# Optimization experiments

Hardware: AMD Instinct MI355X
Metric: run time of the kernel (lower is better)

The kernel has to match this reference:

```python
import jax, jax.numpy as jnp
import numpy as np

B, T, N, IN_DIM = 32, 12, 1024, 1
HID, EMB, K, HOR, OUT = 64, 16, 2, 12, 1


def setup_inputs() -> dict:
    key = jax.random.key(0)
    ks = jax.random.split(key, 12)
    s = 0.1
    return {
        "x": jax.random.normal(ks[0], (B, T, N, IN_DIM), jnp.float32),
        "E": jax.random.normal(ks[1], (N, EMB), jnp.float32),
        # layer 1: gate (z,r) and candidate pools; in = IN_DIM + HID
        "Wg1": jax.random.normal(ks[2], (EMB, K, IN_DIM + HID, 2 * HID), jnp.float32) * s,
        "bg1": jax.random.normal(ks[3], (EMB, 2 * HID), jnp.float32) * s,
        "Wc1": jax.random.normal(ks[4], (EMB, K, IN_DIM + HID, HID), jnp.float32) * s,
        "bc1": jax.random.normal(ks[5], (EMB, HID), jnp.float32) * s,
        # layer 2: in = HID + HID
        "Wg2": jax.random.normal(ks[6], (EMB, K, 2 * HID, 2 * HID), jnp.float32) * s,
        "bg2": jax.random.normal(ks[7], (EMB, 2 * HID), jnp.float32) * s,
        "Wc2": jax.random.normal(ks[8], (EMB, K, 2 * HID, HID), jnp.float32) * s,
        "bc2": jax.random.normal(ks[9], (EMB, HID), jnp.float32) * s,
        # Conv2d(1, HOR*OUT, kernel=(1, HID)) == per-node linear HID -> HOR*OUT
        "Wout": jax.random.normal(ks[10], (HOR * OUT, HID), jnp.float32) * s,
        "bout": jnp.zeros((HOR * OUT,), jnp.float32),
    }


def _supports(E):
    # adaptive adjacency from node embeddings + Chebyshev polynomial set
    A = jax.nn.softmax(jax.nn.relu(E @ E.T), axis=1)  # [N, N]
    sup = [jnp.eye(E.shape[0], dtype=E.dtype), A]
    for _ in range(K - 2):
        sup.append(2.0 * (A @ sup[-1]) - sup[-2])
    return jnp.stack(sup[:K])  # [K, N, N]


def _gconv(x, sup, E, Wp, bp):
    # x: [B, N, Ci]; per-node weights generated from embeddings
    xg = jnp.einsum('knm,bmc->bnkc', sup, x)          # [B, N, K, Ci]
    W = jnp.einsum('nd,dkio->nkio', E, Wp)            # [N, K, Ci, Co]
    b = E @ bp                                        # [N, Co]
    return jnp.einsum('bnki,nkio->bno', xg, W) + b


def _layer(xs, sup, E, Wg, bg, Wc, bc):
    # xs: [T, B, N, Ci]; adaptive graph-conv GRU scanned over time
    hid = Wc.shape[-1]

    def step(h, x_t):
        zr = jax.nn.sigmoid(_gconv(jnp.concatenate([x_t, h], -1), sup, E, Wg, bg))
        z, r = jnp.split(zr, 2, axis=-1)
        hc = jnp.tanh(_gconv(jnp.concatenate([x_t, z * h], -1), sup, E, Wc, bc))
        h_new = r * h + (1.0 - r) * hc
        return h_new, h_new

    h0 = jnp.zeros((xs.shape[1], xs.shape[2], hid), xs.dtype)
    _, hs = jax.lax.scan(step, h0, xs)
    return hs  # [T, B, N, hid]


def reference(x, E, Wg1, bg1, Wc1, bc1, Wg2, bg2, Wc2, bc2, Wout, bout):
    sup = _supports(E)
    xs = jnp.swapaxes(x, 0, 1)                        # [T, B, N, in]
    h1 = _layer(xs, sup, E, Wg1, bg1, Wc1, bc1)       # [T, B, N, HID]
    h2 = _layer(h1, sup, E, Wg2, bg2, Wc2, bc2)       # [T, B, N, HID]
    h_last = h2[-1]                                   # [B, N, HID]
    out = jnp.einsum('bnh,oh->bno', h_last, Wout) + bout  # [B, N, HOR*OUT]
    out = jnp.transpose(out, (0, 2, 1)).reshape(x.shape[0], HOR, OUT, N)
    return jnp.transpose(out, (0, 1, 3, 2))           # [B, HOR, N, OUT]
```

## Files before the change

kernel.cpp:

```cpp
#include <hip/hip_runtime.h>
#include <math.h>

#define NN 1024
#define BB 32
#define TTT 12
#define HH 64
#define DD 16

__device__ __forceinline__ float dot4f(const float4 v, const float* __restrict__ wv) {
    return v.x * wv[0] + v.y * wv[1] + v.z * wv[2] + v.w * wv[3];
}

__device__ __forceinline__ float sigmoidf_(float x) { return 1.0f / (1.0f + expf(-x)); }

__global__ __launch_bounds__(256) void compute_A_kernel(const float* __restrict__ E,
                                                        float* __restrict__ A) {
    int n = blockIdx.x;
    int tid = threadIdx.x;
    __shared__ float en[DD];
    __shared__ float red[256];
    if (tid < DD) en[tid] = E[n * DD + tid];
    __syncthreads();
    float s[4];
    float lmax = 0.0f;
    #pragma unroll
    for (int it = 0; it < 4; ++it) {
        int m = tid + it * 256;
        float acc = 0.0f;
        #pragma unroll
        for (int d = 0; d < DD; ++d) acc += en[d] * E[m * DD + d];
        acc = fmaxf(acc, 0.0f);
        s[it] = acc;
        lmax = fmaxf(lmax, acc);
    }
    red[tid] = lmax; __syncthreads();
    for (int st = 128; st > 0; st >>= 1) {
        if (tid < st) red[tid] = fmaxf(red[tid], red[tid + st]);
        __syncthreads();
    }
    float mx = red[0];
    __syncthreads();
    float lsum = 0.0f;
    #pragma unroll
    for (int it = 0; it < 4; ++it) { s[it] = expf(s[it] - mx); lsum += s[it]; }
    red[tid] = lsum; __syncthreads();
    for (int st = 128; st > 0; st >>= 1) {
        if (tid < st) red[tid] += red[tid + st];
        __syncthreads();
    }
    float inv = 1.0f / red[0];
    #pragma unroll
    for (int it = 0; it < 4; ++it) {
        int m = tid + it * 256;
        A[n * NN + m] = s[it] * inv;
    }
}

__global__ __launch_bounds__(256) void gen_w_f32_kernel(const float* __restrict__ E,
                                                        const float* __restrict__ Wp,
                                                        float* __restrict__ out,
                                                        int rowlen, int total) {
    int idx = blockIdx.x * 256 + threadIdx.x;
    if (idx >= total) return;
    int n = idx / rowlen;
    int j = idx - n * rowlen;
    const float* e = E + n * DD;
    float acc = 0.0f;
    #pragma unroll
    for (int d = 0; d < DD; ++d) acc += e[d] * Wp[d * rowlen + j];
    out[idx] = acc;
}

__global__ __launch_bounds__(256) void transpose_x_kernel(const float* __restrict__ x,
                                                          float* __restrict__ xTm) {
    int idx = blockIdx.x * 256 + threadIdx.x;
    int m = idx / (TTT * BB);
    int tb = idx - m * (TTT * BB);
    int t = tb >> 5;
    int b = tb & 31;
    xTm[idx] = x[(b * TTT + t) * NN + m];
}

__global__ __launch_bounds__(256) void diffuse_gemm(const float* __restrict__ A,
                                                    const float* __restrict__ S,
                                                    float* __restrict__ C, int cols) {
    __shared__ alignas(16) float As[16][68];
    __shared__ alignas(16) float Bs[16][64];
    const int tid = threadIdx.x;
    const int tx = tid & 15, ty = tid >> 4;
    const int rowbase = blockIdx.y * 64, colbase = blockIdx.x * 64;
    const int kl = tid & 15, r0 = (tid >> 4) * 4;
    const int ml = tid >> 6, cl = tid & 63;
    float pa[4], pb[4];
    #pragma unroll
    for (int r = 0; r < 4; ++r)
        pa[r] = A[(size_t)(rowbase + r0 + r) * NN + kl];
    #pragma unroll
    for (int mm = 0; mm < 4; ++mm)
        pb[mm] = S[(size_t)(ml + mm * 4) * cols + colbase + cl];
    float acc[4][4] = {};
    for (int kt = 0; kt < NN; kt += 16) {
        #pragma unroll
        for (int r = 0; r < 4; ++r) As[kl][r0 + r] = pa[r];
        #pragma unroll
        for (int mm = 0; mm < 4; ++mm) Bs[ml + mm * 4][cl] = pb[mm];
        __syncthreads();
        int kn = kt + 16;
        if (kn < NN) {
            #pragma unroll
            for (int r = 0; r < 4; ++r)
                pa[r] = A[(size_t)(rowbase + r0 + r) * NN + kn + kl];
            #pragma unroll
            for (int mm = 0; mm < 4; ++mm)
                pb[mm] = S[(size_t)(kn + ml + mm * 4) * cols + colbase + cl];
        }
        #pragma unroll
        for (int kk = 0; kk < 16; ++kk) {
            float4 a = *(const float4*)&As[kk][ty * 4];
            float4 b = *(const float4*)&Bs[kk][tx * 4];
            acc[0][0] += a.x * b.x; acc[0][1] += a.x * b.y; acc[0][2] += a.x * b.z; acc[0][3] += a.x * b.w;
            acc[1][0] += a.y * b.x; acc[1][1] += a.y * b.y; acc[1][2] += a.y * b.z; acc[1][3] += a.y * b.w;
            acc[2][0] += a.z * b.x; acc[2][1] += a.z * b.y; acc[2][2] += a.z * b.z; acc[2][3] += a.z * b.w;
            acc[3][0] += a.w * b.x; acc[3][1] += a.w * b.y; acc[3][2] += a.w * b.z; acc[3][3] += a.w * b.w;
        }
        __syncthreads();
    }
    #pragma unroll
    for (int i = 0; i < 4; ++i) {
        float4 v = make_float4(acc[i][0], acc[i][1], acc[i][2], acc[i][3]);
        *(float4*)&C[(size_t)(rowbase + ty * 4 + i) * cols + colbase + tx * 4] = v;
    }
}


__global__ __launch_bounds__(256) void l1_gate_fused(int t,
        const float* __restrict__ xTm, const float* __restrict__ AxA,
        const float* __restrict__ h1, const float* __restrict__ Ah1,
        const float* __restrict__ E, const float4* __restrict__ Wp4,
        const float* __restrict__ Bg,
        float* __restrict__ zh, float* __restrict__ rb) {
    int n = blockIdx.x, tid = threadIdx.x;
    __shared__ float en[DD];
    __shared__ alignas(16) float Wl[65 * 128];
    __shared__ alignas(16) float S0[BB * HH];
    __shared__ alignas(16) float S1[BB * HH];
    __shared__ float sx[BB], sax[BB];
    if (tid < DD) en[tid] = E[n * DD + tid];
    for (int i = tid; i < BB * HH; i += 256) {
        S0[i] = h1[(size_t)n * (BB * HH) + i];
        S1[i] = Ah1[(size_t)n * (BB * HH) + i];
    }
    if (tid < BB) sx[tid] = xTm[n * (TTT * BB) + t * BB + tid];
    else if (tid < 2 * BB) sax[tid - BB] = AxA[n * (TTT * BB) + t * BB + (tid - BB)];
    __syncthreads();
    const int o = tid & 63, bq = tid >> 6;
    float accA[8], accB[8];
    float biasA = Bg[n * 128 + o], biasB = Bg[n * 128 + 64 + o];
    #pragma unroll
    for (int j = 0; j < 8; ++j) { accA[j] = biasA; accB[j] = biasB; }
    for (int k = 0; k < 2; ++k) {
        for (int idx = tid; idx < 2080; idx += 256) {
            float4 a = make_float4(0.f, 0.f, 0.f, 0.f);
            #pragma unroll
            for (int d = 0; d < DD; ++d) {
                float ed = en[d];
                float4 w = Wp4[(size_t)d * 4160 + k * 2080 + idx];
                a.x += ed * w.x; a.y += ed * w.y; a.z += ed * w.z; a.w += ed * w.w;
            }
            *(float4*)&Wl[idx * 4] = a;
        }
        __syncthreads();
        const float* S = (k == 0) ? S0 : S1;
        float wxa = Wl[o], wxb = Wl[64 + o];
        #pragma unroll
        for (int j = 0; j < 8; ++j) {
            int b = bq * 8 + j;
            float xv = (k == 0) ? sx[b] : sax[b];
            accA[j] += xv * wxa; accB[j] += xv * wxb;
        }
        for (int i = 0; i < HH; i += 4) {
            float wa[4], wb[4];
            #pragma unroll
            for (int q = 0; q < 4; ++q) {
                int row = (1 + i + q) * 128;
                wa[q] = Wl[row + o]; wb[q] = Wl[row + 64 + o];
            }
            #pragma unroll
            for (int j = 0; j < 8; ++j) {
                int b = bq * 8 + j;
                float4 sv = *(const float4*)&S[b * HH + i];
                accA[j] += dot4f(sv, wa); accB[j] += dot4f(sv, wb);
            }
        }
        __syncthreads();
    }
    #pragma unroll
    for (int j = 0; j < 8; ++j) {
        int b = bq * 8 + j;
        float z = sigmoidf_(accA[j]);
        float r = sigmoidf_(accB[j]);
        zh[(size_t)n * (BB * HH) + b * HH + o] = z * S0[b * HH + o];
        rb[(size_t)n * (BB * HH) + b * HH + o] = r;
    }
}

__global__ __launch_bounds__(256) void l1_cand_fused(int t,
        const float* __restrict__ xTm, const float* __restrict__ AxA,
        const float* __restrict__ zhb, const float* __restrict__ azh,
        const float* __restrict__ E, const float4* __restrict__ Wp4,
        const float* __restrict__ Bc,
        const float* __restrict__ rb, float* __restrict__ h1) {
    int n = blockIdx.x, tid = threadIdx.x;
    __shared__ float en[DD];
    __shared__ alignas(16) float Wl[65 * 64];
    __shared__ alignas(16) float S0[BB * HH];
    __shared__ alignas(16) float S1[BB * HH];
    __shared__ float sx[BB], sax[BB];
    if (tid < DD) en[tid] = E[n * DD + tid];
    for (int i = tid; i < BB * HH; i += 256) {
        S0[i] = zhb[(size_t)n * (BB * HH) + i];
        S1[i] = azh[(size_t)n * (BB * HH) + i];
    }
    if (tid < BB) sx[tid] = xTm[n * (TTT * BB) + t * BB + tid];
    else if (tid < 2 * BB) sax[tid - BB] = AxA[n * (TTT * BB) + t * BB + (tid - BB)];
    __syncthreads();
    const int o = tid & 63, bq = tid >> 6;
    float acc[8];
    float bias = Bc[n * 64 + o];
    #pragma unroll
    for (int j = 0; j < 8; ++j) acc[j] = bias;
    for (int k = 0; k < 2; ++k) {
        for (int idx = tid; idx < 1040; idx += 256) {
            float4 a = make_float4(0.f, 0.f, 0.f, 0.f);
            #pragma unroll
            for (int d = 0; d < DD; ++d) {
                float ed = en[d];
                float4 w = Wp4[(size_t)d * 2080 + k * 1040 + idx];
                a.x += ed * w.x; a.y += ed * w.y; a.z += ed * w.z; a.w += ed * w.w;
            }
            *(float4*)&Wl[idx * 4] = a;
        }
        __syncthreads();
        const float* S = (k == 0) ? S0 : S1;
        float wx = Wl[o];
        #pragma unroll
        for (int j = 0; j < 8; ++j) {
            int b = bq * 8 + j;
            float xv = (k == 0) ? sx[b] : sax[b];
            acc[j] += xv * wx;
        }
        for (int i = 0; i < HH; i += 4) {
            float wa[4];
            #pragma unroll
            for (int q = 0; q < 4; ++q) wa[q] = Wl[(1 + i + q) * 64 + o];
            #pragma unroll
            for (int j = 0; j < 8; ++j) {
                int b = bq * 8 + j;
                float4 sv = *(const float4*)&S[b * HH + i];
                acc[j] += dot4f(sv, wa);
            }
        }
        __syncthreads();
    }
    #pragma unroll
    for (int j = 0; j < 8; ++j) {
        int b = bq * 8 + j;
        size_t idx = (size_t)n * (BB * HH) + b * HH + o;
        float hc = tanhf(acc[j]);
        float r = rb[idx];
        float hold = h1[idx];
        h1[idx] = r * hold + (1.0f - r) * hc;
    }
}

__global__ __launch_bounds__(256) void l2_gate_fused(
        const float* __restrict__ h1, const float* __restrict__ Ah1,
        const float* __restrict__ h2, const float* __restrict__ Ah2,
        const float* __restrict__ E, const float4* __restrict__ Wp4,
        const float* __restrict__ Bg,
        float* __restrict__ zh, float* __restrict__ rb) {
    int n = blockIdx.x, tid = threadIdx.x;
    __shared__ float en[DD];
    __shared__ alignas(16) float Wl[64 * 128];
    __shared__ alignas(16) float Sl[4][BB * HH];
    if (tid < DD) en[tid] = E[n * DD + tid];
    for (int i = tid; i < BB * HH; i += 256) {
        size_t base = (size_t)n * (BB * HH) + i;
        Sl[0][i] = h1[base]; Sl[1][i] = h2[base];
        Sl[2][i] = Ah1[base]; Sl[3][i] = Ah2[base];
    }
    __syncthreads();
    const int o = tid & 63, bq = tid >> 6;
    float accA[8], accB[8];
    float biasA = Bg[n * 128 + o], biasB = Bg[n * 128 + 64 + o];
    #pragma unroll
    for (int j = 0; j < 8; ++j) { accA[j] = biasA; accB[j] = biasB; }
    for (int p = 0; p < 4; ++p) {
        int k = p >> 1, half = p & 1;
        for (int idx = tid; idx < 2048; idx += 256) {
            float4 a = make_float4(0.f, 0.f, 0.f, 0.f);
            #pragma unroll
            for (int d = 0; d < DD; ++d) {
                float ed = en[d];
                float4 w = Wp4[(size_t)d * 8192 + k * 4096 + half * 2048 + idx];
                a.x += ed * w.x; a.y += ed * w.y; a.z += ed * w.z; a.w += ed * w.w;
            }
            *(float4*)&Wl[idx * 4] = a;
        }
        __syncthreads();
        const float* S = Sl[k * 2 + half];
        for (int i = 0; i < HH; i += 4) {
            float wa[4], wb[4];
            #pragma unroll
            for (int q = 0; q < 4; ++q) {
                int row = (i + q) * 128;
                wa[q] = Wl[row + o]; wb[q] = Wl[row + 64 + o];
            }
            #pragma unroll
            for (int j = 0; j < 8; ++j) {
                int b = bq * 8 + j;
                float4 sv = *(const float4*)&S[b * HH + i];
                accA[j] += dot4f(sv, wa); accB[j] += dot4f(sv, wb);
            }
        }
        __syncthreads();
    }
    #pragma unroll
    for (int j = 0; j < 8; ++j) {
        int b = bq * 8 + j;
        float z = sigmoidf_(accA[j]);
        float r = sigmoidf_(accB[j]);
        zh[(size_t)n * (BB * HH) + b * HH + o] = z * Sl[1][b * HH + o];
        rb[(size_t)n * (BB * HH) + b * HH + o] = r;
    }
}

__global__ __launch_bounds__(256) void l2_cand_fused(
        const float* __restrict__ h1, const float* __restrict__ Ah1,
        const float* __restrict__ zhb, const float* __restrict__ azh,
        const float* __restrict__ E, const float4* __restrict__ Wp4,
        const float* __restrict__ Bc,
        const float* __restrict__ rb, float* __restrict__ h2) {
    int n = blockIdx.x, tid = threadIdx.x;
    __shared__ float en[DD];
    __shared__ alignas(16) float Wl[64 * 64];
    __shared__ alignas(16) float Sl[4][BB * HH];
    if (tid < DD) en[tid] = E[n * DD + tid];
    for (int i = tid; i < BB * HH; i += 256) {
        size_t base = (size_t)n * (BB * HH) + i;
        Sl[0][i] = h1[base];  Sl[1][i] = zhb[base];
        Sl[2][i] = Ah1[base]; Sl[3][i] = azh[base];
    }
    __syncthreads();
    const int o = tid & 63, bq = tid >> 6;
    float acc[8];
    float bias = Bc[n * 64 + o];
    #pragma unroll
    for (int j = 0; j < 8; ++j) acc[j] = bias;
    for (int p = 0; p < 4; ++p) {
        int k = p >> 1, half = p & 1;
        for (int idx = tid; idx < 1024; idx += 256) {
            float4 a = make_float4(0.f, 0.f, 0.f, 0.f);
            #pragma unroll
            for (int d = 0; d < DD; ++d) {
                float ed = en[d];
                float4 w = Wp4[(size_t)d * 4096 + k * 2048 + half * 1024 + idx];
                a.x += ed * w.x; a.y += ed * w.y; a.z += ed * w.z; a.w += ed * w.w;
            }
            *(float4*)&Wl[idx * 4] = a;
        }
        __syncthreads();
        const float* S = Sl[k * 2 + half];
        for (int i = 0; i < HH; i += 4) {
            float wa[4];
            #pragma unroll
            for (int q = 0; q < 4; ++q) wa[q] = Wl[(i + q) * 64 + o];
            #pragma unroll
            for (int j = 0; j < 8; ++j) {
                int b = bq * 8 + j;
                float4 sv = *(const float4*)&S[b * HH + i];
                acc[j] += dot4f(sv, wa);
            }
        }
        __syncthreads();
    }
    #pragma unroll
    for (int j = 0; j < 8; ++j) {
        int b = bq * 8 + j;
        size_t idx = (size_t)n * (BB * HH) + b * HH + o;
        float hc = tanhf(acc[j]);
        float r = rb[idx];
        float hold = h2[idx];
        h2[idx] = r * hold + (1.0f - r) * hc;
    }
}

__global__ __launch_bounds__(384) void out_kernel(const float* __restrict__ h2,
                                                  const float* __restrict__ Wout,
                                                  const float* __restrict__ bout,
                                                  float* __restrict__ out) {
    int n = blockIdx.x;
    int tid = threadIdx.x;
    __shared__ float shh[BB * HH];
    __shared__ float sw[TTT * HH];
    __shared__ float sb[TTT];
    for (int i = tid; i < BB * HH; i += 384) shh[i] = h2[(size_t)n * (BB * HH) + i];
    for (int i = tid; i < TTT * HH; i += 384) sw[i] = Wout[i];
    if (tid < TTT) sb[tid] = bout[tid];
    __syncthreads();
    int b = tid & 31;
    int hor = tid >> 5;
    float acc = sb[hor];
    #pragma unroll
    for (int c = 0; c < HH; ++c) acc += shh[b * HH + c] * sw[hor * HH + c];
    out[(size_t)(b * TTT + hor) * NN + n] = acc;
}

__global__ void report_ws_kernel(float* out, float v) { out[0] = v; }

extern "C" void kernel_launch(void* const* d_in, const int* in_sizes, int n_in,
                              void* d_out, int out_size, void* d_ws, size_t ws_size,
                              hipStream_t stream) {
    const float* x    = (const float*)d_in[0];
    const float* E    = (const float*)d_in[1];
    const float* Wg1p = (const float*)d_in[2];
    const float* bg1p = (const float*)d_in[3];
    const float* Wc1p = (const float*)d_in[4];
    const float* bc1p = (const float*)d_in[5];
    const float* Wg2p = (const float*)d_in[6];
    const float* bg2p = (const float*)d_in[7];
    const float* Wc2p = (const float*)d_in[8];
    const float* bc2p = (const float*)d_in[9];
    const float* Wout = (const float*)d_in[10];
    const float* bout = (const float*)d_in[11];
    float* out = (float*)d_out;
    float* ws = (float*)d_ws;

    size_t off = 0;
    float* A_   = ws + off; off += (size_t)NN * NN;
    float* B1g  = ws + off; off += (size_t)NN * 128;
    float* B1c  = ws + off; off += (size_t)NN * 64;
    float* B2g  = ws + off; off += (size_t)NN * 128;
    float* B2c  = ws + off; off += (size_t)NN * 64;
    float* xTm  = ws + off; off += (size_t)NN * TTT * BB;
    float* AxA  = ws + off; off += (size_t)NN * TTT * BB;
    const size_t ST = (size_t)NN * BB * HH;
    float* h1   = ws + off; off += ST;
    float* h2   = ws + off; off += ST;
    float* Ah1  = ws + off; off += ST;
    float* Ah2  = ws + off; off += ST;
    float* Azh  = ws + off; off += ST;
    float* ZH   = ws + off; off += ST;
    float* Rb   = ws + off; off += ST;
    size_t need_bytes = off * sizeof(float);
    if (ws_size < need_bytes) {
        report_ws_kernel<<<1, 1, 0, stream>>>(out, (float)ws_size);
        return;
    }

    (void)hipMemsetAsync(h1, 0, ST * 4, stream);
    (void)hipMemsetAsync(h2, 0, ST * 4, stream);
    (void)hipMemsetAsync(Ah1, 0, ST * 4, stream);
    (void)hipMemsetAsync(Ah2, 0, ST * 4, stream);
    (void)hipMemsetAsync(Azh, 0, ST * 4, stream);

    compute_A_kernel<<<NN, 256, 0, stream>>>(E, A_);
    gen_w_f32_kernel<<<(131072 + 255) / 256, 256, 0, stream>>>(E, bg1p, B1g, 128, 131072);
    gen_w_f32_kernel<<<(65536 + 255) / 256, 256, 0, stream>>>(E, bc1p, B1c, 64, 65536);
    gen_w_f32_kernel<<<(131072 + 255) / 256, 256, 0, stream>>>(E, bg2p, B2g, 128, 131072);
    gen_w_f32_kernel<<<(65536 + 255) / 256, 256, 0, stream>>>(E, bc2p, B2c, 64, 65536);
    transpose_x_kernel<<<(NN * TTT * BB) / 256, 256, 0, stream>>>(x, xTm);
    diffuse_gemm<<<dim3((TTT * BB) / 64, NN / 64), 256, 0, stream>>>(A_, xTm, AxA, TTT * BB);

    const int COLS = BB * HH;
    dim3 gemmGrid(COLS / 64, NN / 64);

    for (int t = 0; t < TTT; ++t) {
        l1_gate_fused<<<NN, 256, 0, stream>>>(t, xTm, AxA, h1, Ah1,
                                              E, (const float4*)Wg1p, B1g, ZH, Rb);
        if (t > 0) diffuse_gemm<<<gemmGrid, 256, 0, stream>>>(A_, ZH, Azh, COLS);
        l1_cand_fused<<<NN, 256, 0, stream>>>(t, xTm, AxA, ZH, Azh,
                                              E, (const float4*)Wc1p, B1c, Rb, h1);
        diffuse_gemm<<<gemmGrid, 256, 0, stream>>>(A_, h1, Ah1, COLS);
        l2_gate_fused<<<NN, 256, 0, stream>>>(h1, Ah1, h2, Ah2,
                                              E, (const float4*)Wg2p, B2g, ZH, Rb);
        if (t > 0) diffuse_gemm<<<gemmGrid, 256, 0, stream>>>(A_, ZH, Azh, COLS);
        l2_cand_fused<<<NN, 256, 0, stream>>>(h1, Ah1, ZH, Azh,
                                              E, (const float4*)Wc2p, B2c, Rb, h2);
        if (t < TTT - 1) diffuse_gemm<<<gemmGrid, 256, 0, stream>>>(A_, h2, Ah2, COLS);
    }

    out_kernel<<<NN, 384, 0, stream>>>(h2, Wout, bout, out);
}
```

Measured before the change: 6.357 ms.

## Double-buffer diffusion GEMM tiles and halve per-node weight staging in LDS

The diffusion GEMM now double-buffers its shared A/B tiles, so each k-step needs one barrier instead of two. The four fused GRU gate and candidate kernels generate their per-node weights in 32-row chunks, with the x-input row held in a small separate buffer. This roughly halves the weight LDS footprint, aiming for more resident blocks per CU. The cost is more chunk passes and barriers per block.

```diff
diff --git a/kernel.cpp b/kernel.cpp
--- a/kernel.cpp
+++ b/kernel.cpp
@@ -84,8 +84,8 @@
 __global__ __launch_bounds__(256) void diffuse_gemm(const float* __restrict__ A,
                                                     const float* __restrict__ S,
                                                     float* __restrict__ C, int cols) {
-    __shared__ alignas(16) float As[16][68];
-    __shared__ alignas(16) float Bs[16][64];
+    __shared__ alignas(16) float As[2][16][68];
+    __shared__ alignas(16) float Bs[2][16][64];
     const int tid = threadIdx.x;
     const int tx = tid & 15, ty = tid >> 4;
     const int rowbase = blockIdx.y * 64, colbase = blockIdx.x * 64;
@@ -98,13 +98,14 @@
     #pragma unroll
     for (int mm = 0; mm < 4; ++mm)
         pb[mm] = S[(size_t)(ml + mm * 4) * cols + colbase + cl];
+    #pragma unroll
+    for (int r = 0; r < 4; ++r) As[0][kl][r0 + r] = pa[r];
+    #pragma unroll
+    for (int mm = 0; mm < 4; ++mm) Bs[0][ml + mm * 4][cl] = pb[mm];
+    __syncthreads();
+    int cur = 0;
     float acc[4][4] = {};
     for (int kt = 0; kt < NN; kt += 16) {
-        #pragma unroll
-        for (int r = 0; r < 4; ++r) As[kl][r0 + r] = pa[r];
-        #pragma unroll
-        for (int mm = 0; mm < 4; ++mm) Bs[ml + mm * 4][cl] = pb[mm];
-        __syncthreads();
         int kn = kt + 16;
         if (kn < NN) {
             #pragma unroll
@@ -116,14 +117,22 @@
         }
         #pragma unroll
         for (int kk = 0; kk < 16; ++kk) {
-            float4 a = *(const float4*)&As[kk][ty * 4];
-            float4 b = *(const float4*)&Bs[kk][tx * 4];
+            float4 a = *(const float4*)&As[cur][kk][ty * 4];
+            float4 b = *(const float4*)&Bs[cur][kk][tx * 4];
             acc[0][0] += a.x * b.x; acc[0][1] += a.x * b.y; acc[0][2] += a.x * b.z; acc[0][3] += a.x * b.w;
             acc[1][0] += a.y * b.x; acc[1][1] += a.y * b.y; acc[1][2] += a.y * b.z; acc[1][3] += a.y * b.w;
             acc[2][0] += a.z * b.x; acc[2][1] += a.z * b.y; acc[2][2] += a.z * b.z; acc[2][3] += a.z * b.w;
             acc[3][0] += a.w * b.x; acc[3][1] += a.w * b.y; acc[3][2] += a.w * b.z; acc[3][3] += a.w * b.w;
         }
-        __syncthreads();
+        if (kn < NN) {
+            int nxt = cur ^ 1;
+            #pragma unroll
+            for (int r = 0; r < 4; ++r) As[nxt][kl][r0 + r] = pa[r];
+            #pragma unroll
+            for (int mm = 0; mm < 4; ++mm) Bs[nxt][ml + mm * 4][cl] = pb[mm];
+            __syncthreads();
+            cur = nxt;
+        }
     }
     #pragma unroll
     for (int i = 0; i < 4; ++i) {
@@ -141,7 +150,8 @@
         float* __restrict__ zh, float* __restrict__ rb) {
     int n = blockIdx.x, tid = threadIdx.x;
     __shared__ float en[DD];
-    __shared__ alignas(16) float Wl[65 * 128];
+    __shared__ alignas(16) float Wx[2 * 128];
+    __shared__ alignas(16) float Wl[32 * 128];
     __shared__ alignas(16) float S0[BB * HH];
     __shared__ alignas(16) float S1[BB * HH];
     __shared__ float sx[BB], sax[BB];
@@ -153,42 +163,59 @@
     if (tid < BB) sx[tid] = xTm[n * (TTT * BB) + t * BB + tid];
     else if (tid < 2 * BB) sax[tid - BB] = AxA[n * (TTT * BB) + t * BB + (tid - BB)];
     __syncthreads();
+    if (tid < 64) {
+        int k = tid >> 5, idx = tid & 31;
+        float4 a = make_float4(0.f, 0.f, 0.f, 0.f);
+        #pragma unroll
+        for (int d = 0; d < DD; ++d) {
+            float ed = en[d];
+            float4 w = Wp4[(size_t)d * 4160 + k * 2080 + idx];
+            a.x += ed * w.x; a.y += ed * w.y; a.z += ed * w.z; a.w += ed * w.w;
+        }
+        *(float4*)&Wx[k * 128 + idx * 4] = a;
+    }
     const int o = tid & 63, bq = tid >> 6;
     float accA[8], accB[8];
     float biasA = Bg[n * 128 + o], biasB = Bg[n * 128 + 64 + o];
     #pragma unroll
     for (int j = 0; j < 8; ++j) { accA[j] = biasA; accB[j] = biasB; }
-    for (int k = 0; k < 2; ++k) {
-        for (int idx = tid; idx < 2080; idx += 256) {
+    for (int p = 0; p < 4; ++p) {
+        int k = p >> 1, half = p & 1;
+        #pragma unroll
+        for (int it = 0; it < 4; ++it) {
+            int idx = tid + it * 256;
             float4 a = make_float4(0.f, 0.f, 0.f, 0.f);
             #pragma unroll
             for (int d = 0; d < DD; ++d) {
                 float ed = en[d];
-                float4 w = Wp4[(size_t)d * 4160 + k * 2080 + idx];
+                float4 w = Wp4[(size_t)d * 4160 + k * 2080 + (1 + half * 32) * 32 + idx];
                 a.x += ed * w.x; a.y += ed * w.y; a.z += ed * w.z; a.w += ed * w.w;
             }
             *(float4*)&Wl[idx * 4] = a;
         }
         __syncthreads();
         const float* S = (k == 0) ? S0 : S1;
-        float wxa = Wl[o], wxb = Wl[64 + o];
-        #pragma unroll
-        for (int j = 0; j < 8; ++j) {
-            int b = bq * 8 + j;
-            float xv = (k == 0) ? sx[b] : sax[b];
-            accA[j] += xv * wxa; accB[j] += xv * wxb;
-        }
-        for (int i = 0; i < HH; i += 4) {
-            float wa[4], wb[4];
-            #pragma unroll
-            for (int q = 0; q < 4; ++q) {
-                int row = (1 + i + q) * 128;
-                wa[q] = Wl[row + o]; wb[q] = Wl[row + 64 + o];
-            }
+        if (half == 0) {
+            float wxa = Wx[k * 128 + o], wxb = Wx[k * 128 + 64 + o];
             #pragma unroll
             for (int j = 0; j < 8; ++j) {
                 int b = bq * 8 + j;
-                float4 sv = *(const float4*)&S[b * HH + i];
+                float xv = (k == 0) ? sx[b] : sax[b];
+                accA[j] += xv * wxa; accB[j] += xv * wxb;
+            }
+        }
+        int ibase = half * 32;
+        for (int i = 0; i < 32; i += 4) {
+            float wa[4], wb[4];
+            #pragma unroll
+            for (int q = 0; q < 4; ++q) {
+                wa[q] = Wl[(i + q) * 128 + o];
+                wb[q] = Wl[(i + q) * 128 + 64 + o];
+            }
+            #pragma unroll
+            for (int j = 0; j < 8; ++j) {
+                int b = bq * 8 + j;
+                float4 sv = *(const float4*)&S[b * HH + ibase + i];
                 accA[j] += dot4f(sv, wa); accB[j] += dot4f(sv, wb);
             }
         }
@@ -212,7 +239,8 @@
         const float* __restrict__ rb, float* __restrict__ h1) {
     int n = blockIdx.x, tid = threadIdx.x;
     __shared__ float en[DD];
-    __shared__ alignas(16) float Wl[65 * 64];
+    __shared__ alignas(16) float Wx[2 * 64];
+    __shared__ alignas(16) float Wl[32 * 64];
     __shared__ alignas(16) float S0[BB * HH];
     __shared__ alignas(16) float S1[BB * HH];
     __shared__ float sx[BB], sax[BB];
@@ -224,39 +252,56 @@
     if (tid < BB) sx[tid] = xTm[n * (TTT * BB) + t * BB + tid];
     else if (tid < 2 * BB) sax[tid - BB] = AxA[n * (TTT * BB) + t * BB + (tid - BB)];
     __syncthreads();
+    if (tid < 32) {
+        int k = tid >> 4, idx = tid & 15;
+        float4 a = make_float4(0.f, 0.f, 0.f, 0.f);
+        #pragma unroll
+        for (int d = 0; d < DD; ++d) {
+            float ed = en[d];
+            float4 w = Wp4[(size_t)d * 2080 + k * 1040 + idx];
+            a.x += ed * w.x; a.y += ed * w.y; a.z += ed * w.z; a.w += ed * w.w;
+        }
+        *(float4*)&Wx[k * 64 + idx * 4] = a;
+    }
     const int o = tid & 63, bq = tid >> 6;
     float acc[8];
     float bias = Bc[n * 64 + o];
     #pragma unroll
     for (int j = 0; j < 8; ++j) acc[j] = bias;
-    for (int k = 0; k < 2; ++k) {
-        for (int idx = tid; idx < 1040; idx += 256) {
+    for (int p = 0; p < 4; ++p) {
+        int k = p >> 1, half = p & 1;
+        #pragma unroll
+        for (int it = 0; it < 2; ++it) {
+            int idx = tid + it * 256;
             float4 a = make_float4(0.f, 0.f, 0.f, 0.f);
             #pragma unroll
             for (int d = 0; d < DD; ++d) {
                 float ed = en[d];
-                float4 w = Wp4[(size_t)d * 2080 + k * 1040 + idx];
+                float4 w = Wp4[(size_t)d * 2080 + k * 1040 + (1 + half * 32) * 16 + idx];
                 a.x += ed * w.x; a.y += ed * w.y; a.z += ed * w.z; a.w += ed * w.w;
             }
             *(float4*)&Wl[idx * 4] = a;
         }
         __syncthreads();
         const float* S = (k == 0) ? S0 : S1;
-        float wx = Wl[o];
-        #pragma unroll
-        for (int j = 0; j < 8; ++j) {
-            int b = bq * 8 + j;
-            float xv = (k == 0) ? sx[b] : sax[b];
-            acc[j] += xv * wx;
-        }
-        for (int i = 0; i < HH; i += 4) {
-            float wa[4];
-            #pragma unroll
-            for (int q = 0; q < 4; ++q) wa[q] = Wl[(1 + i + q) * 64 + o];
+        if (half == 0) {
+            float wx = Wx[k * 64 + o];
             #pragma unroll
             for (int j = 0; j < 8; ++j) {
                 int b = bq * 8 + j;
-                float4 sv = *(const float4*)&S[b * HH + i];
+                float xv = (k == 0) ? sx[b] : sax[b];
+                acc[j] += xv * wx;
+            }
+        }
+        int ibase = half * 32;
+        for (int i = 0; i < 32; i += 4) {
+            float wa[4];
+            #pragma unroll
+            for (int q = 0; q < 4; ++q) wa[q] = Wl[(i + q) * 64 + o];
+            #pragma unroll
+            for (int j = 0; j < 8; ++j) {
+                int b = bq * 8 + j;
+                float4 sv = *(const float4*)&S[b * HH + ibase + i];
                 acc[j] += dot4f(sv, wa);
             }
         }
@@ -281,7 +326,7 @@
         float* __restrict__ zh, float* __restrict__ rb) {
     int n = blockIdx.x, tid = threadIdx.x;
     __shared__ float en[DD];
-    __shared__ alignas(16) float Wl[64 * 128];
+    __shared__ alignas(16) float Wl[32 * 128];
     __shared__ alignas(16) float Sl[4][BB * HH];
     if (tid < DD) en[tid] = E[n * DD + tid];
     for (int i = tid; i < BB * HH; i += 256) {
@@ -295,31 +340,34 @@
     float biasA = Bg[n * 128 + o], biasB = Bg[n * 128 + 64 + o];
     #pragma unroll
     for (int j = 0; j < 8; ++j) { accA[j] = biasA; accB[j] = biasB; }
-    for (int p = 0; p < 4; ++p) {
-        int k = p >> 1, half = p & 1;
-        for (int idx = tid; idx < 2048; idx += 256) {
+    for (int p = 0; p < 8; ++p) {
+        int k = p >> 2, q = p & 3;
+        #pragma unroll
+        for (int it = 0; it < 4; ++it) {
+            int idx = tid + it * 256;
             float4 a = make_float4(0.f, 0.f, 0.f, 0.f);
             #pragma unroll
             for (int d = 0; d < DD; ++d) {
                 float ed = en[d];
-                float4 w = Wp4[(size_t)d * 8192 + k * 4096 + half * 2048 + idx];
+                float4 w = Wp4[(size_t)d * 8192 + k * 4096 + q * 1024 + idx];
                 a.x += ed * w.x; a.y += ed * w.y; a.z += ed * w.z; a.w += ed * w.w;
             }
             *(float4*)&Wl[idx * 4] = a;
         }
         __syncthreads();
-        const float* S = Sl[k * 2 + half];
-        for (int i = 0; i < HH; i += 4) {
+        const float* S = Sl[k * 2 + (q >> 1)];
+        int ibase = (q & 1) * 32;
+        for (int i = 0; i < 32; i += 4) {
             float wa[4], wb[4];
             #pragma unroll
-            for (int q = 0; q < 4; ++q) {
-                int row = (i + q) * 128;
-                wa[q] = Wl[row + o]; wb[q] = Wl[row + 64 + o];
+            for (int qq = 0; qq < 4; ++qq) {
+                wa[qq] = Wl[(i + qq) * 128 + o];
+                wb[qq] = Wl[(i + qq) * 128 + 64 + o];
             }
             #pragma unroll
             for (int j = 0; j < 8; ++j) {
                 int b = bq * 8 + j;
-                float4 sv = *(const float4*)&S[b * HH + i];
+                float4 sv = *(const float4*)&S[b * HH + ibase + i];
                 accA[j] += dot4f(sv, wa); accB[j] += dot4f(sv, wb);
             }
         }
@@ -343,7 +391,7 @@
         const float* __restrict__ rb, float* __restrict__ h2) {
     int n = blockIdx.x, tid = threadIdx.x;
     __shared__ float en[DD];
-    __shared__ alignas(16) float Wl[64 * 64];
+    __shared__ alignas(16) float Wl[32 * 64];
     __shared__ alignas(16) float Sl[4][BB * HH];
     if (tid < DD) en[tid] = E[n * DD + tid];
     for (int i = tid; i < BB * HH; i += 256) {
@@ -357,28 +405,31 @@
     float bias = Bc[n * 64 + o];
     #pragma unroll
     for (int j = 0; j < 8; ++j) acc[j] = bias;
-    for (int p = 0; p < 4; ++p) {
-        int k = p >> 1, half = p & 1;
-        for (int idx = tid; idx < 1024; idx += 256) {
+    for (int p = 0; p < 8; ++p) {
+        int k = p >> 2, q = p & 3;
+        #pragma unroll
+        for (int it = 0; it < 2; ++it) {
+            int idx = tid + it * 256;
             float4 a = make_float4(0.f, 0.f, 0.f, 0.f);
             #pragma unroll
             for (int d = 0; d < DD; ++d) {
                 float ed = en[d];
-                float4 w = Wp4[(size_t)d * 4096 + k * 2048 + half * 1024 + idx];
+                float4 w = Wp4[(size_t)d * 4096 + k * 2048 + q * 512 + idx];
                 a.x += ed * w.x; a.y += ed * w.y; a.z += ed * w.z; a.w += ed * w.w;
             }
             *(float4*)&Wl[idx * 4] = a;
         }
         __syncthreads();
-        const float* S = Sl[k * 2 + half];
-        for (int i = 0; i < HH; i += 4) {
+        const float* S = Sl[k * 2 + (q >> 1)];
+        int ibase = (q & 1) * 32;
+        for (int i = 0; i < 32; i += 4) {
             float wa[4];
             #pragma unroll
-            for (int q = 0; q < 4; ++q) wa[q] = Wl[(i + q) * 64 + o];
+            for (int qq = 0; qq < 4; ++qq) wa[qq] = Wl[(i + qq) * 64 + o];
             #pragma unroll
             for (int j = 0; j < 8; ++j) {
                 int b = bq * 8 + j;
-                float4 sv = *(const float4*)&S[b * HH + i];
+                float4 sv = *(const float4*)&S[b * HH + ibase + i];
                 acc[j] += dot4f(sv, wa);
             }
         }
```

After: 7.393 ms. 1.16x slower.

## Precompute per-node gate weights once and double-buffer diffusion GEMM shared tiles

Applied to the files above, without the earlier changes.

Instead of regenerating the per-node gate weights from the embedding pools inside every timestep's gate kernel, the weights for layer-2 (and layer-1 when workspace allows) are materialized once up front and read directly from global memory. This removes 16-term embedding contractions repeated every step, at the cost of large weight buffers (128 MB plus 68 MB) that are streamed from HBM each step. The diffusion GEMM also gains a double-buffered shared-memory tile, dropping one barrier per k-iteration.

```diff
diff --git a/kernel.cpp b/kernel.cpp
--- a/kernel.cpp
+++ b/kernel.cpp
@@ -71,6 +71,25 @@
     out[idx] = acc;
 }
 
+__global__ __launch_bounds__(256) void gen_w4_kernel(const float* __restrict__ E,
+                                                     const float4* __restrict__ Wp4,
+                                                     float4* __restrict__ out4,
+                                                     int rowlen4, int total4) {
+    int idx = blockIdx.x * 256 + threadIdx.x;
+    if (idx >= total4) return;
+    int n = idx / rowlen4;
+    int j = idx - n * rowlen4;
+    const float* e = E + n * DD;
+    float4 acc = make_float4(0.f, 0.f, 0.f, 0.f);
+    #pragma unroll
+    for (int d = 0; d < DD; ++d) {
+        float ed = e[d];
+        float4 w = Wp4[(size_t)d * rowlen4 + j];
+        acc.x += ed * w.x; acc.y += ed * w.y; acc.z += ed * w.z; acc.w += ed * w.w;
+    }
+    out4[idx] = acc;
+}
+
 __global__ __launch_bounds__(256) void transpose_x_kernel(const float* __restrict__ x,
                                                           float* __restrict__ xTm) {
     int idx = blockIdx.x * 256 + threadIdx.x;
@@ -84,8 +103,8 @@
 __global__ __launch_bounds__(256) void diffuse_gemm(const float* __restrict__ A,
                                                     const float* __restrict__ S,
                                                     float* __restrict__ C, int cols) {
-    __shared__ alignas(16) float As[16][68];
-    __shared__ alignas(16) float Bs[16][64];
+    __shared__ alignas(16) float As[2][16][68];
+    __shared__ alignas(16) float Bs[2][16][64];
     const int tid = threadIdx.x;
     const int tx = tid & 15, ty = tid >> 4;
     const int rowbase = blockIdx.y * 64, colbase = blockIdx.x * 64;
@@ -98,13 +117,14 @@
     #pragma unroll
     for (int mm = 0; mm < 4; ++mm)
         pb[mm] = S[(size_t)(ml + mm * 4) * cols + colbase + cl];
+    #pragma unroll
+    for (int r = 0; r < 4; ++r) As[0][kl][r0 + r] = pa[r];
+    #pragma unroll
+    for (int mm = 0; mm < 4; ++mm) Bs[0][ml + mm * 4][cl] = pb[mm];
+    __syncthreads();
+    int cur = 0;
     float acc[4][4] = {};
     for (int kt = 0; kt < NN; kt += 16) {
-        #pragma unroll
-        for (int r = 0; r < 4; ++r) As[kl][r0 + r] = pa[r];
-        #pragma unroll
-        for (int mm = 0; mm < 4; ++mm) Bs[ml + mm * 4][cl] = pb[mm];
-        __syncthreads();
         int kn = kt + 16;
         if (kn < NN) {
             #pragma unroll
@@ -116,19 +136,142 @@
         }
         #pragma unroll
         for (int kk = 0; kk < 16; ++kk) {
-            float4 a = *(const float4*)&As[kk][ty * 4];
-            float4 b = *(const float4*)&Bs[kk][tx * 4];
+            float4 a = *(const float4*)&As[cur][kk][ty * 4];
+            float4 b = *(const float4*)&Bs[cur][kk][tx * 4];
             acc[0][0] += a.x * b.x; acc[0][1] += a.x * b.y; acc[0][2] += a.x * b.z; acc[0][3] += a.x * b.w;
             acc[1][0] += a.y * b.x; acc[1][1] += a.y * b.y; acc[1][2] += a.y * b.z; acc[1][3] += a.y * b.w;
             acc[2][0] += a.z * b.x; acc[2][1] += a.z * b.y; acc[2][2] += a.z * b.z; acc[2][3] += a.z * b.w;
             acc[3][0] += a.w * b.x; acc[3][1] += a.w * b.y; acc[3][2] += a.w * b.z; acc[3][3] += a.w * b.w;
         }
-        __syncthreads();
+        if (kn < NN) {
+            int nxt = cur ^ 1;
+            #pragma unroll
+            for (int r = 0; r < 4; ++r) As[nxt][kl][r0 + r] = pa[r];
+            #pragma unroll
+            for (int mm = 0; mm < 4; ++mm) Bs[nxt][ml + mm * 4][cl] = pb[mm];
+            __syncthreads();
+            cur = nxt;
+        }
     }
     #pragma unroll
     for (int i = 0; i < 4; ++i) {
         float4 v = make_float4(acc[i][0], acc[i][1], acc[i][2], acc[i][3]);
         *(float4*)&C[(size_t)(rowbase + ty * 4 + i) * cols + colbase + tx * 4] = v;
+    }
+}
+
+
+__global__ __launch_bounds__(256) void l1_gate_kernel(int t,
+        const float* __restrict__ xTm, const float* __restrict__ AxA,
+        const float* __restrict__ h1, const float* __restrict__ Ah1,
+        const float* __restrict__ Wg, const float* __restrict__ Bg,
+        float* __restrict__ zh, float* __restrict__ rb) {
+    int n = blockIdx.x;
+    int tid = threadIdx.x;
+    __shared__ alignas(16) float sh[BB * HH];
+    __shared__ alignas(16) float sa[BB * HH];
+    __shared__ float sx[BB], sax[BB];
+    for (int i = tid; i < BB * HH; i += 256) {
+        sh[i] = h1[(size_t)n * (BB * HH) + i];
+        sa[i] = Ah1[(size_t)n * (BB * HH) + i];
+    }
+    if (tid < BB) sx[tid] = xTm[n * (TTT * BB) + t * BB + tid];
+    else if (tid < 2 * BB) sax[tid - BB] = AxA[n * (TTT * BB) + t * BB + (tid - BB)];
+    __syncthreads();
+    const int o = tid & 63;
+    const int bq = tid >> 6;
+    const float* W = Wg + (size_t)n * 16640;
+    float accA[8], accB[8];
+    float biasA = Bg[n * 128 + o], biasB = Bg[n * 128 + 64 + o];
+    float wxa0 = W[o], wxa1 = W[8320 + o];
+    float wxb0 = W[64 + o], wxb1 = W[8320 + 64 + o];
+    #pragma unroll
+    for (int j = 0; j < 8; ++j) {
+        int b = bq * 8 + j;
+        accA[j] = biasA + sx[b] * wxa0 + sax[b] * wxa1;
+        accB[j] = biasB + sx[b] * wxb0 + sax[b] * wxb1;
+    }
+    for (int i = 0; i < HH; i += 4) {
+        float w0a[4], w1a[4], w0b[4], w1b[4];
+        #pragma unroll
+        for (int q = 0; q < 4; ++q) {
+            int row = (1 + i + q) * 128;
+            w0a[q] = W[row + o];            w1a[q] = W[8320 + row + o];
+            w0b[q] = W[row + 64 + o];       w1b[q] = W[8320 + row + 64 + o];
+        }
+        #pragma unroll
+        for (int j = 0; j < 8; ++j) {
+            int b = bq * 8 + j;
+            float4 hv = *(const float4*)&sh[b * HH + i];
+            float4 av = *(const float4*)&sa[b * HH + i];
+            accA[j] += dot4f(hv, w0a) + dot4f(av, w1a);
+            accB[j] += dot4f(hv, w0b) + dot4f(av, w1b);
+        }
+    }
+    #pragma unroll
+    for (int j = 0; j < 8; ++j) {
+        int b = bq * 8 + j;
+        float z = sigmoidf_(accA[j]);
+        float r = sigmoidf_(accB[j]);
+        zh[(size_t)n * (BB * HH) + b * HH + o] = z * sh[b * HH + o];
+        rb[(size_t)n * (BB * HH) + b * HH + o] = r;
+    }
+}
+
+__global__ __launch_bounds__(256) void l2_gate_kernel(
+        const float* __restrict__ h1, const float* __restrict__ Ah1,
+        const float* __restrict__ h2, const float* __restrict__ Ah2,
+        const float* __restrict__ Wg, const float* __restrict__ Bg,
+        float* __restrict__ zh, float* __restrict__ rb) {
+    int n = blockIdx.x;
+    int tid = threadIdx.x;
+    __shared__ alignas(16) float s1[BB * HH];
+    __shared__ alignas(16) float sa1[BB * HH];
+    __shared__ alignas(16) float s2[BB * HH];
+    __shared__ alignas(16) float sa2[BB * HH];
+    for (int i = tid; i < BB * HH; i += 256) {
+        size_t base = (size_t)n * (BB * HH) + i;
+        s1[i] = h1[base]; sa1[i] = Ah1[base];
+        s2[i] = h2[base]; sa2[i] = Ah2[base];
+    }
+    __syncthreads();
+    const int o = tid & 63;
+    const int bq = tid >> 6;
+    const float* W = Wg + (size_t)n * 32768;
+    float accA[8], accB[8];
+    float biasA = Bg[n * 128 + o], biasB = Bg[n * 128 + 64 + o];
+    #pragma unroll
+    for (int j = 0; j < 8; ++j) { accA[j] = biasA; accB[j] = biasB; }
+    for (int i = 0; i < HH; i += 4) {
+        float w10a[4], w11a[4], w20a[4], w21a[4];
+        float w10b[4], w11b[4], w20b[4], w21b[4];
+        #pragma unroll
+        for (int q = 0; q < 4; ++q) {
+            int r1 = (i + q) * 128;
+            int r2 = (64 + i + q) * 128;
+            w10a[q] = W[r1 + o];          w10b[q] = W[r1 + 64 + o];
+            w11a[q] = W[16384 + r1 + o];  w11b[q] = W[16384 + r1 + 64 + o];
+            w20a[q] = W[r2 + o];          w20b[q] = W[r2 + 64 + o];
+            w21a[q] = W[16384 + r2 + o];  w21b[q] = W[16384 + r2 + 64 + o];
+        }
+        #pragma unroll
+        for (int j = 0; j < 8; ++j) {
+            int b = bq * 8 + j;
+            float4 v1 = *(const float4*)&s1[b * HH + i];
+            float4 u1 = *(const float4*)&sa1[b * HH + i];
+            float4 v2 = *(const float4*)&s2[b * HH + i];
+            float4 u2 = *(const float4*)&sa2[b * HH + i];
+            accA[j] += dot4f(v1, w10a) + dot4f(u1, w11a) + dot4f(v2, w20a) + dot4f(u2, w21a);
+            accB[j] += dot4f(v1, w10b) + dot4f(u1, w11b) + dot4f(v2, w20b) + dot4f(u2, w21b);
+        }
+    }
+    #pragma unroll
+    for (int j = 0; j < 8; ++j) {
+        int b = bq * 8 + j;
+        float z = sigmoidf_(accA[j]);
+        float r = sigmoidf_(accB[j]);
+        zh[(size_t)n * (BB * HH) + b * HH + o] = z * s2[b * HH + o];
+        rb[(size_t)n * (BB * HH) + b * HH + o] = r;
     }
 }
 
@@ -273,68 +416,6 @@
     }
 }
 
-__global__ __launch_bounds__(256) void l2_gate_fused(
-        const float* __restrict__ h1, const float* __restrict__ Ah1,
-        const float* __restrict__ h2, const float* __restrict__ Ah2,
-        const float* __restrict__ E, const float4* __restrict__ Wp4,
-        const float* __restrict__ Bg,
-        float* __restrict__ zh, float* __restrict__ rb) {
-    int n = blockIdx.x, tid = threadIdx.x;
-    __shared__ float en[DD];
-    __shared__ alignas(16) float Wl[64 * 128];
-    __shared__ alignas(16) float Sl[4][BB * HH];
-    if (tid < DD) en[tid] = E[n * DD + tid];
-    for (int i = tid; i < BB * HH; i += 256) {
-        size_t base = (size_t)n * (BB * HH) + i;
-        Sl[0][i] = h1[base]; Sl[1][i] = h2[base];
-        Sl[2][i] = Ah1[base]; Sl[3][i] = Ah2[base];
-    }
-    __syncthreads();
-    const int o = tid & 63, bq = tid >> 6;
-    float accA[8], accB[8];
-    float biasA = Bg[n * 128 + o], biasB = Bg[n * 128 + 64 + o];
-    #pragma unroll
-    for (int j = 0; j < 8; ++j) { accA[j] = biasA; accB[j] = biasB; }
-    for (int p = 0; p < 4; ++p) {
-        int k = p >> 1, half = p & 1;
-        for (int idx = tid; idx < 2048; idx += 256) {
-            float4 a = make_float4(0.f, 0.f, 0.f, 0.f);
-            #pragma unroll
-            for (int d = 0; d < DD; ++d) {
-                float ed = en[d];
-                float4 w = Wp4[(size_t)d * 8192 + k * 4096 + half * 2048 + idx];
-                a.x += ed * w.x; a.y += ed * w.y; a.z += ed * w.z; a.w += ed * w.w;
-            }
-            *(float4*)&Wl[idx * 4] = a;
-        }
-        __syncthreads();
-        const float* S = Sl[k * 2 + half];
-        for (int i = 0; i < HH; i += 4) {
-            float wa[4], wb[4];
-            #pragma unroll
-            for (int q = 0; q < 4; ++q) {
-                int row = (i + q) * 128;
-                wa[q] = Wl[row + o]; wb[q] = Wl[row + 64 + o];
-            }
-            #pragma unroll
-            for (int j = 0; j < 8; ++j) {
-                int b = bq * 8 + j;
-                float4 sv = *(const float4*)&S[b * HH + i];
-                accA[j] += dot4f(sv, wa); accB[j] += dot4f(sv, wb);
-            }
-        }
-        __syncthreads();
-    }
-    #pragma unroll
-    for (int j = 0; j < 8; ++j) {
-        int b = bq * 8 + j;
-        float z = sigmoidf_(accA[j]);
-        float r = sigmoidf_(accB[j]);
-        zh[(size_t)n * (BB * HH) + b * HH + o] = z * Sl[1][b * HH + o];
-        rb[(size_t)n * (BB * HH) + b * HH + o] = r;
-    }
-}
-
 __global__ __launch_bounds__(256) void l2_cand_fused(
         const float* __restrict__ h1, const float* __restrict__ Ah1,
         const float* __restrict__ zhb, const float* __restrict__ azh,
@@ -374,7 +455,7 @@
         for (int i = 0; i < HH; i += 4) {
             float wa[4];
             #pragma unroll
-            for (int q = 0; q < 4; ++q) wa[q] = Wl[(i + q) * 64 + o];
+            for (int qq = 0; qq < 4; ++qq) wa[qq] = Wl[(i + qq) * 64 + o];
             #pragma unroll
             for (int j = 0; j < 8; ++j) {
                 int b = bq * 8 + j;
@@ -452,11 +533,15 @@
     float* Azh  = ws + off; off += ST;
     float* ZH   = ws + off; off += ST;
     float* Rb   = ws + off; off += ST;
-    size_t need_bytes = off * sizeof(float);
-    if (ws_size < need_bytes) {
+    float* W2G  = ws + off; off += (size_t)NN * 32768;
+    size_t need_w2g = off * sizeof(float);
+    float* W1G  = ws + off;
+    size_t need_w1g = need_w2g + (size_t)NN * 16640 * sizeof(float);
+    if (ws_size < need_w2g) {
         report_ws_kernel<<<1, 1, 0, stream>>>(out, (float)ws_size);
         return;
     }
+    const bool w1g_static = (ws_size >= need_w1g);
 
     (void)hipMemsetAsync(h1, 0, ST * 4, stream);
     (void)hipMemsetAsync(h2, 0, ST * 4, stream);
@@ -471,19 +556,27 @@
     gen_w_f32_kernel<<<(65536 + 255) / 256, 256, 0, stream>>>(E, bc2p, B2c, 64, 65536);
     transpose_x_kernel<<<(NN * TTT * BB) / 256, 256, 0, stream>>>(x, xTm);
     diffuse_gemm<<<dim3((TTT * BB) / 64, NN / 64), 256, 0, stream>>>(A_, xTm, AxA, TTT * BB);
+    gen_w4_kernel<<<(8388608 + 255) / 256, 256, 0, stream>>>(
+        E, (const float4*)Wg2p, (float4*)W2G, 8192, 8388608);
+    if (w1g_static) {
+        gen_w4_kernel<<<(4259840 + 255) / 256, 256, 0, stream>>>(
+            E, (const float4*)Wg1p, (float4*)W1G, 4160, 4259840);
+    }
 
     const int COLS = BB * HH;
     dim3 gemmGrid(COLS / 64, NN / 64);
 
     for (int t = 0; t < TTT; ++t) {
-        l1_gate_fused<<<NN, 256, 0, stream>>>(t, xTm, AxA, h1, Ah1,
-                                              E, (const float4*)Wg1p, B1g, ZH, Rb);
+        if (w1g_static)
+            l1_gate_kernel<<<NN, 256, 0, stream>>>(t, xTm, AxA, h1, Ah1, W1G, B1g, ZH, Rb);
+        else
+            l1_gate_fused<<<NN, 256, 0, stream>>>(t, xTm, AxA, h1, Ah1,
+                                                  E, (const float4*)Wg1p, B1g, ZH, Rb);
         if (t > 0) diffuse_gemm<<<gemmGrid, 256, 0, stream>>>(A_, ZH, Azh, COLS);
         l1_cand_fused<<<NN, 256, 0, stream>>>(t, xTm, AxA, ZH, Azh,
                                               E, (const float4*)Wc1p, B1c, Rb, h1);
         diffuse_gemm<<<gemmGrid, 256, 0, stream>>>(A_, h1, Ah1, COLS);
-        l2_gate_fused<<<NN, 256, 0, stream>>>(h1, Ah1, h2, Ah2,
-                                              E, (const float4*)Wg2p, B2g, ZH, Rb);
+        l2_gate_kernel<<<NN, 256, 0, stream>>>(h1, Ah1, h2, Ah2, W2G, B2g, ZH, Rb);
         if (t > 0) diffuse_gemm<<<gemmGrid, 256, 0, stream>>>(A_, ZH, Azh, COLS);
         l2_cand_fused<<<NN, 256, 0, stream>>>(h1, Ah1, ZH, Azh,
                                               E, (const float4*)Wc2p, B2c, Rb, h2);
```

After: 5.891 ms. 7.3% less time.
